# Kernel tuning notes

Hardware: AMD Instinct MI355X
Metric: run time of the kernel (lower is better)

Reference implementation:

```python
import jax, jax.numpy as jnp
import numpy as np

N = 50000
E = 800000
F_IN, H1, H2, C = 512, 256, 32, 16


def _glorot(key, shape):
    lim = float(np.sqrt(6.0 / (shape[0] + shape[1])))
    return jax.random.uniform(key, shape, jnp.float32, -lim, lim)


def setup_inputs() -> dict:
    key = jax.random.key(0)
    ks = jax.random.split(key, 8)
    x = jax.random.normal(ks[0], (N, F_IN), jnp.float32)
    edge_index = jax.random.randint(ks[1], (2, E), 0, N, jnp.int64)
    return {
        "x": x,
        "edge_index": edge_index,
        "W1": _glorot(ks[2], (F_IN, H1)), "b1": jnp.zeros((H1,), jnp.float32),
        "W2": _glorot(ks[3], (H1, H2)), "b2": jnp.zeros((H2,), jnp.float32),
        "W3": _glorot(ks[4], (H2, C)), "b3": jnp.zeros((C,), jnp.float32),
    }


def _gcn_norm(edge_index, n_nodes):
    # Add self-loops, compute symmetric normalization deg^-1/2[src]*deg^-1/2[dst]
    loop = jnp.arange(n_nodes, dtype=edge_index.dtype)
    src = jnp.concatenate([edge_index[0], loop])
    dst = jnp.concatenate([edge_index[1], loop])
    ones = jnp.ones(src.shape[0], jnp.float32)
    deg = jax.ops.segment_sum(ones, dst, num_segments=n_nodes)
    dinv = jnp.where(deg > 0, jax.lax.rsqrt(deg), 0.0)
    norm = dinv[src] * dinv[dst]  # [E+N]
    return src, dst, norm


def _gcn_conv(x, W, b, src, dst, norm, n_nodes):
    h = x @ W  # transform first (reduces scatter width)
    msg = h[src] * norm[:, None]  # gather + scale, [E+N, out]
    out = jax.ops.segment_sum(msg, dst, num_segments=n_nodes)
    return out + b


def reference(x, edge_index, W1, b1, W2, b2, W3, b3):
    n_nodes = x.shape[0]
    src, dst, norm = _gcn_norm(edge_index, n_nodes)
    h = _gcn_conv(x, W1, b1, src, dst, norm, n_nodes)
    h = jax.nn.relu(h)  # dropout is identity in eval mode
    h = _gcn_conv(h, W2, b2, src, dst, norm, n_nodes)
    h = jax.nn.relu(h)
    h = _gcn_conv(h, W3, b3, src, dst, norm, n_nodes)
    return h
```

## Files before the change

kernel.cpp:

```cpp
#include <hip/hip_runtime.h>

constexpr int N   = 50000;
constexpr int E   = 800000;
constexpr int FIN = 512;
constexpr int H1v = 256;
constexpr int H2v = 32;
constexpr int Cv  = 16;

constexpr int NBLK = (N + 1023) / 1024;

typedef __attribute__((ext_vector_type(8))) short short8;
typedef __attribute__((ext_vector_type(4))) float f32x4;
typedef __attribute__((ext_vector_type(4))) unsigned short us4;

__device__ inline unsigned short f2bf(float f) {
    unsigned u = __float_as_uint(f);
    return (unsigned short)((u + 0x7FFFu + ((u >> 16) & 1u)) >> 16);
}
__device__ inline float bf2f(unsigned short b) { return __uint_as_float(((unsigned)b) << 16); }


__global__ __launch_bounds__(256) void k_hist(const int* __restrict__ dst,
                                              int* __restrict__ cnt) {
    int e = blockIdx.x * 256 + threadIdx.x;
    if (e < E) atomicAdd(&cnt[dst[e]], 1);
}

__global__ __launch_bounds__(256) void k_scan_part(const int* __restrict__ cnt,
                                                   int* __restrict__ bsum) {
    __shared__ int red[256];
    const int t = threadIdx.x;
    const int base = blockIdx.x * 1024 + t * 4;
    int s = 0;
#pragma unroll
    for (int i = 0; i < 4; ++i) {
        int idx = base + i;
        if (idx < N) s += cnt[idx];
    }
    red[t] = s;
    __syncthreads();
    for (int off = 128; off > 0; off >>= 1) {
        if (t < off) red[t] += red[t + off];
        __syncthreads();
    }
    if (t == 0) bsum[blockIdx.x] = red[0];
}

__global__ __launch_bounds__(64) void k_scan_top(const int* __restrict__ bsum,
                                                 int* __restrict__ boff,
                                                 int* __restrict__ row_ptr) {
    const int l = threadIdx.x;
    int orig = (l < NBLK) ? bsum[l] : 0;
    int v = orig;
    for (int off = 1; off < 64; off <<= 1) {
        int u = __shfl_up(v, off, 64);
        if (l >= off) v += u;
    }
    if (l < NBLK) boff[l] = v - orig;
    if (l == NBLK - 1) row_ptr[N] = v;
}

__global__ __launch_bounds__(256) void k_scan_final(const int* __restrict__ cnt,
                                                    const int* __restrict__ boff,
                                                    int* __restrict__ row_ptr,
                                                    int* __restrict__ cursor,
                                                    float* __restrict__ dinv) {
    __shared__ int sums[256];
    const int t = threadIdx.x;
    const int base = blockIdx.x * 1024 + t * 4;
    int v[4];
    int local = 0;
#pragma unroll
    for (int i = 0; i < 4; ++i) {
        int idx = base + i;
        v[i] = (idx < N) ? cnt[idx] : 0;
        local += v[i];
    }
    sums[t] = local;
    __syncthreads();
    for (int off = 1; off < 256; off <<= 1) {
        int u = (t >= off) ? sums[t - off] : 0;
        __syncthreads();
        sums[t] += u;
        __syncthreads();
    }
    int run = boff[blockIdx.x] + sums[t] - local;
#pragma unroll
    for (int i = 0; i < 4; ++i) {
        int idx = base + i;
        if (idx < N) {
            row_ptr[idx] = run;
            cursor[idx] = run;
            dinv[idx] = rsqrtf(1.0f + (float)v[i]);
        }
        run += v[i];
    }
}

__global__ __launch_bounds__(256) void k_permute(const int* __restrict__ src,
                                                 const int* __restrict__ dst,
                                                 int* __restrict__ cursor,
                                                 int* __restrict__ srcs) {
    int e = blockIdx.x * 256 + threadIdx.x;
    if (e < E) {
        int pos = atomicAdd(&cursor[dst[e]], 1);
        srcs[pos] = src[e];
    }
}


__global__ __launch_bounds__(256) void k_wsplit(const float* __restrict__ W,
                                                unsigned short* __restrict__ Wf) {
    int t = blockIdx.x * 256 + threadIdx.x;
    int l = t & 63, nt = (t >> 6) & 15, kt = t >> 10;
    int n = nt * 16 + (l & 15);
    int kb = kt * 32 + (l >> 4) * 8;
    short8 h8, l8;
#pragma unroll
    for (int j = 0; j < 8; ++j) {
        float w = W[(size_t)(kb + j) * H1v + n];
        unsigned short h = f2bf(w);
        h8[j] = (short)h;
        l8[j] = (short)f2bf(w - bf2f(h));
    }
    size_t base = ((size_t)(kt * 16 + nt) * 2) * 512 + (size_t)l * 8;
    *(short8*)(Wf + base) = h8;
    *(short8*)(Wf + base + 512) = l8;
}


__global__ __launch_bounds__(256, 2) void k_gemm1_mfma(const float* __restrict__ X,
                                                       const unsigned short* __restrict__ Wf,
                                                       const float* __restrict__ dinv,
                                                       unsigned short* __restrict__ Hout) {
    __shared__ char lds[65536];
    const int tid = threadIdx.x;
    const int w = tid >> 6, l = tid & 63;
    const int wr = w >> 1, wc = w & 1;
    const int row0 = blockIdx.x * 128;
    const int colb = blockIdx.y;

    const int arow_l = tid >> 1;
    const int akh = tid & 1;
    const int arow = row0 + arow_l;
    const bool aok = arow < N;
    const float* aptr = X + (size_t)arow * FIN + akh * 32;
    const int art = arow_l >> 4, am = arow_l & 15;

    f32x4 acc[4][4];
#pragma unroll
    for (int i = 0; i < 4; ++i)
#pragma unroll
        for (int j = 0; j < 4; ++j) acc[i][j] = (f32x4)0.f;

    float4 xv[8];
#pragma unroll
    for (int g = 0; g < 8; ++g)
        xv[g] = aok ? *(const float4*)(aptr + g * 4) : make_float4(0.f, 0.f, 0.f, 0.f);

    for (int it = 0; it < 8; ++it) {
        __syncthreads();

#pragma unroll
        for (int c = 0; c < 8; ++c) {
            int chunk = w * 8 + c;
            int plane = chunk & 1, nt = (chunk >> 1) & 7, kt = chunk >> 4;
            int ktg = it * 2 + kt, ntg = colb * 8 + nt;
            const unsigned short* gp = Wf + ((size_t)(ktg * 16 + ntg) * 2 + plane) * 512 + (size_t)l * 8;
            char* lp = lds + 32768 + ((kt * 8 + nt) * 2 + plane) * 1024 + l * 16;
            __builtin_amdgcn_global_load_lds(
                (const __attribute__((address_space(1))) unsigned int*)gp,
                (__attribute__((address_space(3))) unsigned int*)lp, 16, 0, 0);
        }

#pragma unroll
        for (int g = 0; g < 4; ++g) {
            float xs[8] = {xv[2*g].x, xv[2*g].y, xv[2*g].z, xv[2*g].w,
                           xv[2*g+1].x, xv[2*g+1].y, xv[2*g+1].z, xv[2*g+1].w};
            short8 h8, l8;
#pragma unroll
            for (int j = 0; j < 8; ++j) {
                unsigned short h = f2bf(xs[j]);
                h8[j] = (short)h;
                l8[j] = (short)f2bf(xs[j] - bf2f(h));
            }
            char* pa = lds + ((akh * 8 + art) * 2) * 1024 + (g * 16 + am) * 16;
            *(short8*)pa = h8;
            *(short8*)(pa + 1024) = l8;
        }
        __syncthreads();

        if (it < 7) {
#pragma unroll
            for (int g = 0; g < 8; ++g)
                xv[g] = aok ? *(const float4*)(aptr + (it + 1) * 64 + g * 4)
                            : make_float4(0.f, 0.f, 0.f, 0.f);
        }

#pragma unroll
        for (int kt = 0; kt < 2; ++kt) {
            short8 Ah[4], Al[4], Bh[4], Bl[4];
#pragma unroll
            for (int i = 0; i < 4; ++i) {
                char* p = lds + ((kt * 8 + wr * 4 + i) * 2) * 1024 + l * 16;
                Ah[i] = *(short8*)p;
                Al[i] = *(short8*)(p + 1024);
            }
#pragma unroll
            for (int j = 0; j < 4; ++j) {
                char* p = lds + 32768 + ((kt * 8 + wc * 4 + j) * 2) * 1024 + l * 16;
                Bh[j] = *(short8*)p;
                Bl[j] = *(short8*)(p + 1024);
            }
#pragma unroll
            for (int i = 0; i < 4; ++i)
#pragma unroll
                for (int j = 0; j < 4; ++j) {
                    acc[i][j] = __builtin_amdgcn_mfma_f32_16x16x32_bf16(Ah[i], Bh[j], acc[i][j], 0, 0, 0);
                    acc[i][j] = __builtin_amdgcn_mfma_f32_16x16x32_bf16(Ah[i], Bl[j], acc[i][j], 0, 0, 0);
                    acc[i][j] = __builtin_amdgcn_mfma_f32_16x16x32_bf16(Al[i], Bh[j], acc[i][j], 0, 0, 0);
                }
        }
    }

    const int col0 = colb * 128;
#pragma unroll
    for (int i = 0; i < 4; ++i) {
        int rbase = row0 + (wr * 4 + i) * 16 + (l >> 4) * 4;
        float dv[4];
        bool ok[4];
#pragma unroll
        for (int r = 0; r < 4; ++r) {
            int rr = rbase + r;
            ok[r] = rr < N;
            dv[r] = ok[r] ? dinv[rr] : 0.f;
        }
#pragma unroll
        for (int j = 0; j < 4; ++j) {
            int col = col0 + (wc * 4 + j) * 16 + (l & 15);
#pragma unroll
            for (int r = 0; r < 4; ++r)
                if (ok[r]) Hout[(size_t)(rbase + r) * H1v + col] = f2bf(acc[i][j][r] * dv[r]);
        }
    }
}


__global__ __launch_bounds__(256) void k_gemm2(const float* __restrict__ A,
                                               const float* __restrict__ W,
                                               const float* __restrict__ dinv,
                                               unsigned short* __restrict__ Hout) {
    __shared__ float Ws[H1v * H2v];
    const int tid = threadIdx.x;
#pragma unroll
    for (int i = 0; i < 8; ++i) {
        int off = tid * 4 + i * 1024;
        *(float4*)(&Ws[off]) = *(const float4*)(W + off);
    }
    __syncthreads();

    const int row = blockIdx.x * 8 + (tid >> 5);
    const int col = tid & 31;
    if (row >= N) return;
    const float* arow = A + (size_t)row * H1v;
    float sum = 0.f;
#pragma unroll 4
    for (int k = 0; k < H1v; k += 4) {
        float4 a4 = *(const float4*)(arow + k);
        sum = fmaf(a4.x, Ws[(k + 0) * H2v + col], sum);
        sum = fmaf(a4.y, Ws[(k + 1) * H2v + col], sum);
        sum = fmaf(a4.z, Ws[(k + 2) * H2v + col], sum);
        sum = fmaf(a4.w, Ws[(k + 3) * H2v + col], sum);
    }
    Hout[(size_t)row * H2v + col] = f2bf(sum * dinv[row]);
}


__global__ __launch_bounds__(256) void k_gemm3(const float* __restrict__ A,
                                               const float* __restrict__ W,
                                               const float* __restrict__ dinv,
                                               unsigned short* __restrict__ Hout) {
    __shared__ float Ws[H2v * Cv];
    const int tid = threadIdx.x;
    *(float2*)(&Ws[tid * 2]) = *(const float2*)(W + tid * 2);
    __syncthreads();

    const int row = blockIdx.x * 16 + (tid >> 4);
    const int col = tid & 15;
    if (row >= N) return;
    const float* arow = A + (size_t)row * H2v;
    float sum = 0.f;
#pragma unroll
    for (int k = 0; k < H2v; ++k) sum = fmaf(arow[k], Ws[k * Cv + col], sum);
    Hout[(size_t)row * Cv + col] = f2bf(sum * dinv[row]);
}


__global__ __launch_bounds__(256) void k_agg_d256(const unsigned short* __restrict__ h,
                                                  const int* __restrict__ rp,
                                                  const int* __restrict__ srcs,
                                                  const float* __restrict__ dinv,
                                                  const float* __restrict__ bias,
                                                  float* __restrict__ out) {
    const int wave = threadIdx.x >> 6;
    const int lane = threadIdx.x & 63;
    const int d = blockIdx.x * 4 + wave;
    if (d >= N) return;
    const int beg = rp[d], end = rp[d + 1];
    const int fo = lane * 4;
    us4 sv = *(const us4*)(h + (size_t)d * H1v + fo);
    float ax = bf2f(sv.x), ay = bf2f(sv.y), az = bf2f(sv.z), aw = bf2f(sv.w);
    int j = beg;
    for (; j + 3 < end; j += 4) {
        int s0 = srcs[j], s1 = srcs[j + 1], s2 = srcs[j + 2], s3 = srcs[j + 3];
        us4 v0 = *(const us4*)(h + (size_t)s0 * H1v + fo);
        us4 v1 = *(const us4*)(h + (size_t)s1 * H1v + fo);
        us4 v2 = *(const us4*)(h + (size_t)s2 * H1v + fo);
        us4 v3 = *(const us4*)(h + (size_t)s3 * H1v + fo);
        ax += bf2f(v0.x) + bf2f(v1.x) + bf2f(v2.x) + bf2f(v3.x);
        ay += bf2f(v0.y) + bf2f(v1.y) + bf2f(v2.y) + bf2f(v3.y);
        az += bf2f(v0.z) + bf2f(v1.z) + bf2f(v2.z) + bf2f(v3.z);
        aw += bf2f(v0.w) + bf2f(v1.w) + bf2f(v2.w) + bf2f(v3.w);
    }
    for (; j < end; ++j) {
        us4 v = *(const us4*)(h + (size_t)srcs[j] * H1v + fo);
        ax += bf2f(v.x); ay += bf2f(v.y); az += bf2f(v.z); aw += bf2f(v.w);
    }
    const float di = dinv[d];
    const float4 b4 = *(const float4*)(bias + fo);
    float4 o;
    o.x = fmaxf(fmaf(di, ax, b4.x), 0.f);
    o.y = fmaxf(fmaf(di, ay, b4.y), 0.f);
    o.z = fmaxf(fmaf(di, az, b4.z), 0.f);
    o.w = fmaxf(fmaf(di, aw, b4.w), 0.f);
    *(float4*)(out + (size_t)d * H1v + fo) = o;
}

template <int D, bool RELU>
__global__ __launch_bounds__(256) void k_agg_small(const unsigned short* __restrict__ h,
                                                   const int* __restrict__ rp,
                                                   const int* __restrict__ srcs,
                                                   const float* __restrict__ dinv,
                                                   const float* __restrict__ bias,
                                                   float* __restrict__ out) {
    constexpr int PER = 256 / D;
    const int sub = threadIdx.x / D;
    const int f = threadIdx.x % D;
    const int d = blockIdx.x * PER + sub;
    if (d >= N) return;
    const int beg = rp[d], end = rp[d + 1];
    float acc = bf2f(h[(size_t)d * D + f]);
    int j = beg;
    for (; j + 3 < end; j += 4) {
        float v0 = bf2f(h[(size_t)srcs[j] * D + f]);
        float v1 = bf2f(h[(size_t)srcs[j + 1] * D + f]);
        float v2 = bf2f(h[(size_t)srcs[j + 2] * D + f]);
        float v3 = bf2f(h[(size_t)srcs[j + 3] * D + f]);
        acc += v0 + v1 + v2 + v3;
    }
    for (; j < end; ++j) acc += bf2f(h[(size_t)srcs[j] * D + f]);
    float v = fmaf(dinv[d], acc, bias[f]);
    if (RELU) v = fmaxf(v, 0.f);
    out[(size_t)d * D + f] = v;
}


extern "C" void kernel_launch(void* const* d_in, const int* in_sizes, int n_in,
                              void* d_out, int out_size, void* d_ws, size_t ws_size,
                              hipStream_t stream) {
    const float* x  = (const float*)d_in[0];
    const int*   ei = (const int*)d_in[1];
    const float* W1 = (const float*)d_in[2];
    const float* b1 = (const float*)d_in[3];
    const float* W2 = (const float*)d_in[4];
    const float* b2 = (const float*)d_in[5];
    const float* W3 = (const float*)d_in[6];
    const float* b3 = (const float*)d_in[7];
    const int* src = ei;
    const int* dst = ei + E;
    float* out = (float*)d_out;

    char* ws = (char*)d_ws;
    float* dinv   = (float*)ws;
    int*   cnt    = (int*)(ws + 0x40000);
    int*   rp     = cnt;
    int*   cursor = (int*)(ws + 0x80000);
    int*   bsum   = (int*)(ws + 0xB2000);
    int*   boff   = (int*)(ws + 0xB3000);
    int*   srcs   = (int*)(ws + 0xC0000);
    unsigned short* wsplit = (unsigned short*)(ws + (size_t)4 * 1024 * 1024);
    char* p = ws + (size_t)5 * 1024 * 1024;
    unsigned short* h1 = (unsigned short*)p; p += (size_t)N * H1v * sizeof(unsigned short);
    float*          a1 = (float*)p;          p += (size_t)N * H1v * sizeof(float);
    unsigned short* h2 = (unsigned short*)p; p += (size_t)N * H2v * sizeof(unsigned short);
    float*          a2 = (float*)p;          p += (size_t)N * H2v * sizeof(float);
    unsigned short* h3 = (unsigned short*)p;

    hipMemsetAsync(cnt, 0, (N + 1) * sizeof(int), stream);
    k_hist<<<(E + 255) / 256, 256, 0, stream>>>(dst, cnt);
    k_scan_part<<<NBLK, 256, 0, stream>>>(cnt, bsum);
    k_scan_top<<<1, 64, 0, stream>>>(bsum, boff, rp);
    k_scan_final<<<NBLK, 256, 0, stream>>>(cnt, boff, rp, cursor, dinv);
    k_permute<<<(E + 255) / 256, 256, 0, stream>>>(src, dst, cursor, srcs);
    k_wsplit<<<64, 256, 0, stream>>>(W1, wsplit);

    dim3 g1((N + 127) / 128, 2);
    k_gemm1_mfma<<<g1, 256, 0, stream>>>(x, wsplit, dinv, h1);
    k_agg_d256<<<(N + 3) / 4, 256, 0, stream>>>(h1, rp, srcs, dinv, b1, a1);

    k_gemm2<<<N / 8, 256, 0, stream>>>(a1, W2, dinv, h2);
    k_agg_small<32, true><<<N / 8, 256, 0, stream>>>(h2, rp, srcs, dinv, b2, a2);

    k_gemm3<<<N / 16, 256, 0, stream>>>(a2, W3, dinv, h3);
    k_agg_small<16, false><<<N / 16, 256, 0, stream>>>(h3, rp, srcs, dinv, b3, out);
}
```

Baseline: 467.0 us.

## Drop LDS staging in GEMM1; load MFMA fragments directly from global

Rewrites the first-layer MFMA GEMM so each wave loads its A rows and its pre-split B fragments straight from global memory into registers, with no shared-memory staging and no block barriers. The fp32-to-bf16 hi/lo split now truncates and packs pairs with perm instructions instead of rounding element by element. This removes LDS traffic and synchronisation, but the two waves sharing a column tile both fetch the same B data and the two sharing a row tile both fetch the same X rows, so global and L2 traffic grows. The hi part is now truncated rather than rounded, which changes the bf16x3 error slightly.

New measurement: 475.0 us. About the same (+1.7%).

```diff
diff --git a/kernel.cpp b/kernel.cpp
--- a/kernel.cpp
+++ b/kernel.cpp
@@ -12,6 +12,7 @@
 typedef __attribute__((ext_vector_type(8))) short short8;
 typedef __attribute__((ext_vector_type(4))) float f32x4;
 typedef __attribute__((ext_vector_type(4))) unsigned short us4;
+typedef __attribute__((ext_vector_type(4))) unsigned int uint4v;
 
 __device__ inline unsigned short f2bf(float f) {
     unsigned u = __float_as_uint(f);
@@ -129,23 +130,49 @@
 }
 
 
+__device__ inline void split_pair(float x0, float x1, unsigned& hp, unsigned& lp) {
+    unsigned u0 = __float_as_uint(x0), u1 = __float_as_uint(x1);
+    unsigned h0 = u0 & 0xffff0000u, h1 = u1 & 0xffff0000u;
+    float l0 = x0 - __uint_as_float(h0);
+    float l1 = x1 - __uint_as_float(h1);
+    hp = __builtin_amdgcn_perm(u1, u0, 0x07060302u);
+    lp = __builtin_amdgcn_perm(__float_as_uint(l1), __float_as_uint(l0), 0x07060302u);
+}
+
+__device__ inline void split_frag(const float4& a, const float4& b, short8& hi, short8& lo) {
+    unsigned h0, h1, h2, h3, l0, l1, l2, l3;
+    split_pair(a.x, a.y, h0, l0);
+    split_pair(a.z, a.w, h1, l1);
+    split_pair(b.x, b.y, h2, l2);
+    split_pair(b.z, b.w, h3, l3);
+    uint4v h, l;
+    h[0] = h0; h[1] = h1; h[2] = h2; h[3] = h3;
+    l[0] = l0; l[1] = l1; l[2] = l2; l[3] = l3;
+    hi = __builtin_bit_cast(short8, h);
+    lo = __builtin_bit_cast(short8, l);
+}
+
 __global__ __launch_bounds__(256, 2) void k_gemm1_mfma(const float* __restrict__ X,
                                                        const unsigned short* __restrict__ Wf,
                                                        const float* __restrict__ dinv,
                                                        unsigned short* __restrict__ Hout) {
-    __shared__ char lds[65536];
     const int tid = threadIdx.x;
     const int w = tid >> 6, l = tid & 63;
     const int wr = w >> 1, wc = w & 1;
-    const int row0 = blockIdx.x * 128;
+    const int row0 = blockIdx.x * 128 + wr * 64;
     const int colb = blockIdx.y;
-
-    const int arow_l = tid >> 1;
-    const int akh = tid & 1;
-    const int arow = row0 + arow_l;
-    const bool aok = arow < N;
-    const float* aptr = X + (size_t)arow * FIN + akh * 32;
-    const int art = arow_l >> 4, am = arow_l & 15;
+    const int lm = l & 15;
+    const int lk = (l >> 4) * 8;
+
+    const float* ap[4];
+    bool ok[4];
+#pragma unroll
+    for (int i = 0; i < 4; ++i) {
+        int r = row0 + i * 16 + lm;
+        ok[i] = r < N;
+        ap[i] = X + (size_t)r * FIN + lk;
+    }
+    const unsigned short* bp0 = Wf + (size_t)(colb * 8 + wc * 4) * 1024 + (size_t)l * 8;
 
     f32x4 acc[4][4];
 #pragma unroll
@@ -153,94 +180,63 @@
 #pragma unroll
         for (int j = 0; j < 4; ++j) acc[i][j] = (f32x4)0.f;
 
-    float4 xv[8];
-#pragma unroll
-    for (int g = 0; g < 8; ++g)
-        xv[g] = aok ? *(const float4*)(aptr + g * 4) : make_float4(0.f, 0.f, 0.f, 0.f);
-
-    for (int it = 0; it < 8; ++it) {
-        __syncthreads();
-
-#pragma unroll
-        for (int c = 0; c < 8; ++c) {
-            int chunk = w * 8 + c;
-            int plane = chunk & 1, nt = (chunk >> 1) & 7, kt = chunk >> 4;
-            int ktg = it * 2 + kt, ntg = colb * 8 + nt;
-            const unsigned short* gp = Wf + ((size_t)(ktg * 16 + ntg) * 2 + plane) * 512 + (size_t)l * 8;
-            char* lp = lds + 32768 + ((kt * 8 + nt) * 2 + plane) * 1024 + l * 16;
-            __builtin_amdgcn_global_load_lds(
-                (const __attribute__((address_space(1))) unsigned int*)gp,
-                (__attribute__((address_space(3))) unsigned int*)lp, 16, 0, 0);
+    float4 a0[4], a1[4];
+#pragma unroll
+    for (int i = 0; i < 4; ++i) {
+        a0[i] = ok[i] ? *(const float4*)(ap[i]) : make_float4(0.f, 0.f, 0.f, 0.f);
+        a1[i] = ok[i] ? *(const float4*)(ap[i] + 4) : make_float4(0.f, 0.f, 0.f, 0.f);
+    }
+
+    for (int ktg = 0; ktg < 16; ++ktg) {
+        const unsigned short* bp = bp0 + (size_t)ktg * 16384;
+        short8 Bh[4], Bl[4];
+#pragma unroll
+        for (int j = 0; j < 4; ++j) {
+            Bh[j] = *(const short8*)(bp + j * 1024);
+            Bl[j] = *(const short8*)(bp + j * 1024 + 512);
         }
 
-#pragma unroll
-        for (int g = 0; g < 4; ++g) {
-            float xs[8] = {xv[2*g].x, xv[2*g].y, xv[2*g].z, xv[2*g].w,
-                           xv[2*g+1].x, xv[2*g+1].y, xv[2*g+1].z, xv[2*g+1].w};
-            short8 h8, l8;
-#pragma unroll
-            for (int j = 0; j < 8; ++j) {
-                unsigned short h = f2bf(xs[j]);
-                h8[j] = (short)h;
-                l8[j] = (short)f2bf(xs[j] - bf2f(h));
+        short8 Ah[4], Al[4];
+#pragma unroll
+        for (int i = 0; i < 4; ++i) split_frag(a0[i], a1[i], Ah[i], Al[i]);
+
+        if (ktg < 15) {
+#pragma unroll
+            for (int i = 0; i < 4; ++i) {
+                const float* p = ap[i] + (ktg + 1) * 32;
+                a0[i] = ok[i] ? *(const float4*)(p) : make_float4(0.f, 0.f, 0.f, 0.f);
+                a1[i] = ok[i] ? *(const float4*)(p + 4) : make_float4(0.f, 0.f, 0.f, 0.f);
             }
-            char* pa = lds + ((akh * 8 + art) * 2) * 1024 + (g * 16 + am) * 16;
-            *(short8*)pa = h8;
-            *(short8*)(pa + 1024) = l8;
         }
-        __syncthreads();
-
-        if (it < 7) {
-#pragma unroll
-            for (int g = 0; g < 8; ++g)
-                xv[g] = aok ? *(const float4*)(aptr + (it + 1) * 64 + g * 4)
-                            : make_float4(0.f, 0.f, 0.f, 0.f);
-        }
-
-#pragma unroll
-        for (int kt = 0; kt < 2; ++kt) {
-            short8 Ah[4], Al[4], Bh[4], Bl[4];
-#pragma unroll
-            for (int i = 0; i < 4; ++i) {
-                char* p = lds + ((kt * 8 + wr * 4 + i) * 2) * 1024 + l * 16;
-                Ah[i] = *(short8*)p;
-                Al[i] = *(short8*)(p + 1024);
+
+#pragma unroll
+        for (int i = 0; i < 4; ++i)
+#pragma unroll
+            for (int j = 0; j < 4; ++j) {
+                acc[i][j] = __builtin_amdgcn_mfma_f32_16x16x32_bf16(Ah[i], Bh[j], acc[i][j], 0, 0, 0);
+                acc[i][j] = __builtin_amdgcn_mfma_f32_16x16x32_bf16(Ah[i], Bl[j], acc[i][j], 0, 0, 0);
+                acc[i][j] = __builtin_amdgcn_mfma_f32_16x16x32_bf16(Al[i], Bh[j], acc[i][j], 0, 0, 0);
             }
-#pragma unroll
-            for (int j = 0; j < 4; ++j) {
-                char* p = lds + 32768 + ((kt * 8 + wc * 4 + j) * 2) * 1024 + l * 16;
-                Bh[j] = *(short8*)p;
-                Bl[j] = *(short8*)(p + 1024);
-            }
-#pragma unroll
-            for (int i = 0; i < 4; ++i)
-#pragma unroll
-                for (int j = 0; j < 4; ++j) {
-                    acc[i][j] = __builtin_amdgcn_mfma_f32_16x16x32_bf16(Ah[i], Bh[j], acc[i][j], 0, 0, 0);
-                    acc[i][j] = __builtin_amdgcn_mfma_f32_16x16x32_bf16(Ah[i], Bl[j], acc[i][j], 0, 0, 0);
-                    acc[i][j] = __builtin_amdgcn_mfma_f32_16x16x32_bf16(Al[i], Bh[j], acc[i][j], 0, 0, 0);
-                }
-        }
     }
 
     const int col0 = colb * 128;
 #pragma unroll
     for (int i = 0; i < 4; ++i) {
-        int rbase = row0 + (wr * 4 + i) * 16 + (l >> 4) * 4;
+        int rbase = row0 + i * 16 + (l >> 4) * 4;
         float dv[4];
-        bool ok[4];
+        bool okr[4];
 #pragma unroll
         for (int r = 0; r < 4; ++r) {
             int rr = rbase + r;
-            ok[r] = rr < N;
-            dv[r] = ok[r] ? dinv[rr] : 0.f;
+            okr[r] = rr < N;
+            dv[r] = okr[r] ? dinv[rr] : 0.f;
         }
 #pragma unroll
         for (int j = 0; j < 4; ++j) {
-            int col = col0 + (wc * 4 + j) * 16 + (l & 15);
+            int col = col0 + (wc * 4 + j) * 16 + lm;
 #pragma unroll
             for (int r = 0; r < 4; ++r)
-                if (ok[r]) Hout[(size_t)(rbase + r) * H1v + col] = f2bf(acc[i][j][r] * dv[r]);
+                if (okr[r]) Hout[(size_t)(rbase + r) * H1v + col] = f2bf(acc[i][j][r] * dv[r]);
         }
     }
 }
@@ -396,7 +392,7 @@
     float*          a2 = (float*)p;          p += (size_t)N * H2v * sizeof(float);
     unsigned short* h3 = (unsigned short*)p;
 
-    hipMemsetAsync(cnt, 0, (N + 1) * sizeof(int), stream);
+    (void)hipMemsetAsync(cnt, 0, (N + 1) * sizeof(int), stream);
     k_hist<<<(E + 255) / 256, 256, 0, stream>>>(dst, cnt);
     k_scan_part<<<NBLK, 256, 0, stream>>>(cnt, bsum);
     k_scan_top<<<1, 64, 0, stream>>>(bsum, boff, rp);
```
